# Kernel tuning notes

Hardware: AMD Instinct MI355X
Metric: run time of the kernel (lower is better)

The kernel has to match this reference:

```python
import jax, jax.numpy as jnp
import numpy as np

N = 100000
E = 1600000
H = 128


def setup_inputs() -> dict:
    key = jax.random.key(0)
    ks = jax.random.split(key, 9)
    s = 1.0 / np.sqrt(H)
    x = jax.random.normal(ks[0], (N, H), dtype=jnp.float32)
    edge_index = jax.random.randint(ks[1], (2, E), 0, N, dtype=jnp.int64)
    W1l = jax.random.uniform(ks[2], (H, H), jnp.float32, -s, s)
    b1l = jax.random.uniform(ks[3], (H,), jnp.float32, -s, s)
    W1r = jax.random.uniform(ks[4], (H, H), jnp.float32, -s, s)
    W2l = jax.random.uniform(ks[5], (H, H), jnp.float32, -s, s)
    b2l = jax.random.uniform(ks[6], (H,), jnp.float32, -s, s)
    W2r = jax.random.uniform(ks[7], (H, H), jnp.float32, -s, s)
    return {"x": x, "edge_index": edge_index, "W1l": W1l, "b1l": b1l,
            "W1r": W1r, "W2l": W2l, "b2l": b2l, "W2r": W2r}


def _sage(x, src, dst, Wl, bl, Wr):
    # mean-aggregate source features at destination nodes (PyG SAGEConv default)
    n = x.shape[0]
    msg = x[src]                                             # [E, H]
    summed = jax.ops.segment_sum(msg, dst, num_segments=n)   # [N, H]
    cnt = jax.ops.segment_sum(jnp.ones((src.shape[0],), x.dtype), dst,
                              num_segments=n)
    mean = summed / jnp.maximum(cnt, 1.0)[:, None]
    # out = lin_l(mean) + lin_r(x); bias only on lin_l
    return mean @ Wl.T + bl + x @ Wr.T


def reference(x, edge_index, W1l, b1l, W1r, W2l, b2l, W2r):
    src, dst = edge_index[0], edge_index[1]
    h1 = jax.nn.relu(_sage(x, src, dst, W1l, b1l, W1r))
    return _sage(h1, src, dst, W2l, b2l, W2r)
```

## Files before the change

kernel.cpp:

```cpp
#include <hip/hip_runtime.h>

#define N_NODES 100000
#define N_EDGES 1600000
#define H 128

#define NB 391
#define P1_EPB 4096
#define P1_BLOCKS ((N_EDGES + P1_EPB - 1) / P1_EPB)
#define P2_CAP 6144

typedef unsigned short u16;
typedef unsigned int u32;
typedef short bf16x8 __attribute__((ext_vector_type(8)));
typedef float f32x4 __attribute__((ext_vector_type(4)));

static __device__ __forceinline__ u16 f2bf(float f) {
    u32 u = __float_as_uint(f);
    u += 0x7fffu + ((u >> 16) & 1u);
    return (u16)(u >> 16);
}


__global__ void zero_ints(int* __restrict__ p, int n) {
    int i = blockIdx.x * blockDim.x + threadIdx.x;
    if (i < n) p[i] = 0;
}

__global__ __launch_bounds__(1024) void bucket_count(
    const int* __restrict__ dst, int* __restrict__ gcount)
{
    __shared__ int s_cnt[NB];
    const int t = threadIdx.x;
    const int e0 = blockIdx.x * P1_EPB;
    const int ecnt = min(P1_EPB, N_EDGES - e0);
    for (int i = t; i < NB; i += 1024) s_cnt[i] = 0;
    __syncthreads();
    for (int i = t; i < ecnt; i += 1024)
        atomicAdd(&s_cnt[dst[e0 + i] >> 8], 1);
    __syncthreads();
    for (int i = t; i < NB; i += 1024)
        if (s_cnt[i] > 0) atomicAdd(&gcount[i], s_cnt[i]);
}

__global__ __launch_bounds__(512) void bucket_scan(
    const int* __restrict__ gcount, int* __restrict__ bstart, int* __restrict__ bcur)
{
    __shared__ int s[512];
    int t = threadIdx.x;
    int v = (t < NB) ? gcount[t] : 0;
    s[t] = v;
    __syncthreads();
    for (int off = 1; off < 512; off <<= 1) {
        int add = (t >= off) ? s[t - off] : 0;
        __syncthreads();
        s[t] += add;
        __syncthreads();
    }
    if (t < NB) {
        int excl = s[t] - v;
        bstart[t] = excl;
        bcur[t] = excl;
    }
    if (t == NB - 1) bstart[NB] = s[t];
}

__global__ __launch_bounds__(1024) void p1_bin(
    const int* __restrict__ src, const int* __restrict__ dst,
    int* __restrict__ bcur, u32* __restrict__ csrp)
{
    __shared__ int s_cnt[NB];
    __shared__ int s_lstart[NB];
    __shared__ int s_gbase[NB];
    __shared__ int s_scan[512];
    __shared__ u32 s_val[P1_EPB];
    __shared__ u32 s_gaddr[P1_EPB];

    const int t = threadIdx.x;
    const int e0 = blockIdx.x * P1_EPB;
    const int ecnt = min(P1_EPB, N_EDGES - e0);

    for (int i = t; i < NB; i += 1024) s_cnt[i] = 0;
    __syncthreads();
    for (int i = t; i < ecnt; i += 1024)
        atomicAdd(&s_cnt[dst[e0 + i] >> 8], 1);
    __syncthreads();

    int v = (t < NB) ? s_cnt[t] : 0;
    if (t < 512) s_scan[t] = v;
    __syncthreads();
    for (int off = 1; off < 512; off <<= 1) {
        int add = (t < 512 && t >= off) ? s_scan[t - off] : 0;
        __syncthreads();
        if (t < 512) s_scan[t] += add;
        __syncthreads();
    }
    if (t < NB) {
        int ls = s_scan[t] - v;
        s_lstart[t] = ls;
        s_gbase[t] = (v > 0) ? atomicAdd(&bcur[t], v) : 0;
        s_cnt[t] = ls;
    }
    __syncthreads();

    for (int i = t; i < ecnt; i += 1024) {
        int d = dst[e0 + i];
        int s = src[e0 + i];
        int b = d >> 8;
        int slot = atomicAdd(&s_cnt[b], 1);
        s_val[slot]   = ((u32)(d & 255) << 17) | (u32)s;
        s_gaddr[slot] = (u32)(s_gbase[b] + (slot - s_lstart[b]));
    }
    __syncthreads();
    for (int i = t; i < ecnt; i += 1024)
        csrp[s_gaddr[i]] = s_val[i];
}

__global__ __launch_bounds__(1024) void p2_scatter(
    const int* __restrict__ bstart, int* __restrict__ rowstart,
    int* __restrict__ deg, int* __restrict__ csr)
{
    __shared__ u32 s_in[P2_CAP];
    __shared__ u32 s_out[P2_CAP];
    __shared__ int s_cnt[256];
    __shared__ int s_loc[256];
    const int b = blockIdx.x;
    const int t = threadIdx.x;
    const int n0 = b << 8;
    const int s0 = bstart[b];
    const int s1 = bstart[b + 1];
    const int cnt = s1 - s0;

    if (t < 256) s_cnt[t] = 0;
    __syncthreads();
    for (int i = t; i < cnt; i += 1024) {
        u32 p = (u32)csr[s0 + i];
        s_in[i] = p;
        atomicAdd(&s_cnt[p >> 17], 1);
    }
    __syncthreads();
    if (t < 256) s_loc[t] = s_cnt[t];
    __syncthreads();
    for (int off = 1; off < 256; off <<= 1) {
        int add = (t < 256 && t >= off) ? s_loc[t - off] : 0;
        __syncthreads();
        if (t < 256) s_loc[t] += add;
        __syncthreads();
    }
    if (t < 256) {
        int node = n0 + t;
        int excl = s_loc[t] - s_cnt[t];
        if (node < N_NODES) {
            rowstart[node] = s0 + excl;
            deg[node]      = s_cnt[t];
        }
        s_loc[t] = excl;
    }
    __syncthreads();
    for (int i = t; i < cnt; i += 1024) {
        u32 p = s_in[i];
        int pos = atomicAdd(&s_loc[p >> 17], 1);
        s_out[pos] = p & 0x1FFFFu;
    }
    __syncthreads();
    for (int i = t; i < cnt; i += 1024)
        csr[s0 + i] = (int)s_out[i];
}


__global__ __launch_bounds__(256) void cast_x(const float* __restrict__ in,
                                              u16* __restrict__ out) {
    int i = blockIdx.x * 256 + threadIdx.x;
    const float4 v0 = *(const float4*)(in + (size_t)i * 8);
    const float4 v1 = *(const float4*)(in + (size_t)i * 8 + 4);
    u16 o[8];
    o[0]=f2bf(v0.x); o[1]=f2bf(v0.y); o[2]=f2bf(v0.z); o[3]=f2bf(v0.w);
    o[4]=f2bf(v1.x); o[5]=f2bf(v1.y); o[6]=f2bf(v1.z); o[7]=f2bf(v1.w);
    *(bf16x8*)(out + (size_t)i * 8) = *(bf16x8*)o;
}

__global__ __launch_bounds__(256) void cast_w(const float* __restrict__ w1l,
                                              const float* __restrict__ w1r,
                                              const float* __restrict__ w2l,
                                              const float* __restrict__ w2r,
                                              u16* __restrict__ out) {
    int i = blockIdx.x * 256 + threadIdx.x;
    int mat = i >> 14, idx = i & 16383;
    const float* s = (mat == 0) ? w1l : (mat == 1) ? w1r : (mat == 2) ? w2l : w2r;
    out[i] = f2bf(s[idx]);
}


__global__ __launch_bounds__(256) void agg_bf16(
    const u16* __restrict__ xin, const int* __restrict__ csr,
    const int* __restrict__ rowstart, const int* __restrict__ deg,
    u16* __restrict__ mout)
{
    int w = (blockIdx.x * blockDim.x + threadIdx.x) >> 6;
    if (w >= N_NODES) return;
    int lane = threadIdx.x & 63;
    int beg = __builtin_amdgcn_readfirstlane(rowstart[w]);
    int d   = __builtin_amdgcn_readfirstlane(deg[w]);
    const u16* base = xin + (lane << 1);

    float ax[8], ay[8];
#pragma unroll
    for (int u = 0; u < 8; ++u) { ax[u] = 0.f; ay[u] = 0.f; }

    int i = 0;
    for (; i + 8 <= d; i += 8) {
        int s[8];
#pragma unroll
        for (int u = 0; u < 8; ++u) s[u] = csr[beg + i + u];
#pragma unroll
        for (int u = 0; u < 8; ++u) {
            u32 v = *(const u32*)(base + ((size_t)s[u] << 7));
            ax[u] += __uint_as_float(v << 16);
            ay[u] += __uint_as_float(v & 0xffff0000u);
        }
    }
    if (i < d) {
        int cnt = d - i;
        int s[8];
#pragma unroll
        for (int u = 0; u < 8; ++u) s[u] = csr[beg + i + ((u < cnt) ? u : 0)];
#pragma unroll
        for (int u = 0; u < 8; ++u) {
            u32 v = *(const u32*)(base + ((size_t)s[u] << 7));
            if (u < cnt) {
                ax[u] += __uint_as_float(v << 16);
                ay[u] += __uint_as_float(v & 0xffff0000u);
            }
        }
    }

#pragma unroll
    for (int u = 0; u < 4; ++u) { ax[u] += ax[u + 4]; ay[u] += ay[u + 4]; }
    ax[0] += ax[2]; ay[0] += ay[2];
    ax[1] += ax[3]; ay[1] += ay[3];
    ax[0] += ax[1]; ay[0] += ay[1];

    float inv = 1.f / (float)(d > 0 ? d : 1);
    u32 packed = (u32)f2bf(ax[0] * inv) | ((u32)f2bf(ay[0] * inv) << 16);
    *(u32*)(mout + ((size_t)w << 7) + (lane << 1)) = packed;
}

__global__ __launch_bounds__(256) void gemm_mfma4(
    const u16* __restrict__ Ab, const u16* __restrict__ Xb,
    const u16* __restrict__ Wlb, const float* __restrict__ bl,
    const u16* __restrict__ Wrb, void* __restrict__ outp, int relu_bf16)
{
    __shared__ u16 lds[32768];
    const int t  = threadIdx.x;
    const int wv = t >> 6;
    const int l  = t & 63;
    const int lr = l & 15;
    const int lq = l >> 4;
    const int r0 = blockIdx.x * 128;

    bf16x8 bwl[2][4], bwr[2][4];
#pragma unroll
    for (int ct = 0; ct < 2; ++ct) {
        const u16* wl = Wlb + (size_t)(wv * 32 + ct * 16 + lr) * H + lq * 8;
        const u16* wr = Wrb + (size_t)(wv * 32 + ct * 16 + lr) * H + lq * 8;
#pragma unroll
        for (int k0 = 0; k0 < 4; ++k0) {
            bwl[ct][k0] = *(const bf16x8*)(wl + k0 * 32);
            bwr[ct][k0] = *(const bf16x8*)(wr + k0 * 32);
        }
    }
    float bv[2] = { bl[wv * 32 + lr], bl[wv * 32 + 16 + lr] };

    const char* ag = (const char*)(Ab + (size_t)r0 * H);
    const char* xg = (const char*)(Xb + (size_t)r0 * H);
#pragma unroll
    for (int c = 0; c < 8; ++c) {
        int boff = wv * 8192 + c * 1024;
        __builtin_amdgcn_global_load_lds(
            (const u32*)(ag + boff + (l << 4)), (u32*)&lds[boff >> 1], 16, 0, 0);
        __builtin_amdgcn_global_load_lds(
            (const u32*)(xg + boff + (l << 4)), (u32*)&lds[(32768 + boff) >> 1], 16, 0, 0);
    }
    __syncthreads();

    f32x4 acc[8][2];
#pragma unroll
    for (int rt = 0; rt < 8; ++rt) {
        bf16x8 af[4], xf[4];
#pragma unroll
        for (int k0 = 0; k0 < 4; ++k0) {
            int idx = (rt * 16 + lr) * 128 + k0 * 32 + lq * 8;
            af[k0] = *(const bf16x8*)&lds[idx];
            xf[k0] = *(const bf16x8*)&lds[16384 + idx];
        }
#pragma unroll
        for (int ct = 0; ct < 2; ++ct) {
            f32x4 a = (f32x4)0.f;
#pragma unroll
            for (int k0 = 0; k0 < 4; ++k0) {
                a = __builtin_amdgcn_mfma_f32_16x16x32_bf16(af[k0], bwl[ct][k0], a, 0, 0, 0);
                a = __builtin_amdgcn_mfma_f32_16x16x32_bf16(xf[k0], bwr[ct][k0], a, 0, 0, 0);
            }
            acc[rt][ct] = a;
        }
    }
    __syncthreads();

    if (relu_bf16) {
#pragma unroll
        for (int rt = 0; rt < 8; ++rt)
#pragma unroll
        for (int ct = 0; ct < 2; ++ct)
#pragma unroll
        for (int r = 0; r < 4; ++r)
            lds[(rt * 16 + lq * 4 + r) * 128 + wv * 32 + ct * 16 + lr] =
                f2bf(fmaxf(acc[rt][ct][r] + bv[ct], 0.f));
        __syncthreads();
        u16* ob = (u16*)outp;
#pragma unroll
        for (int c = 0; c < 8; ++c) {
            int eoff = c * 2048 + t * 8;
            int row = r0 + (eoff >> 7);
            if (row < N_NODES)
                *(bf16x8*)(ob + (size_t)r0 * H + eoff) = *(const bf16x8*)&lds[eoff];
        }
    } else {
        float* of = (float*)lds;
#pragma unroll
        for (int rt = 0; rt < 8; ++rt)
#pragma unroll
        for (int ct = 0; ct < 2; ++ct)
#pragma unroll
        for (int r = 0; r < 4; ++r)
            of[(rt * 16 + lq * 4 + r) * 128 + wv * 32 + ct * 16 + lr] =
                acc[rt][ct][r] + bv[ct];
        __syncthreads();
        float* og = (float*)outp;
#pragma unroll
        for (int c = 0; c < 16; ++c) {
            int eoff = c * 1024 + t * 4;
            int row = r0 + (eoff >> 7);
            if (row < N_NODES)
                *(float4*)(og + (size_t)r0 * H + eoff) = *(const float4*)&of[eoff];
        }
    }
}


extern "C" void kernel_launch(void* const* d_in, const int* in_sizes, int n_in,
                              void* d_out, int out_size, void* d_ws, size_t ws_size,
                              hipStream_t stream) {
    const float* x   = (const float*)d_in[0];
    const int*   ei  = (const int*)d_in[1];
    const float* W1l = (const float*)d_in[2];
    const float* b1l = (const float*)d_in[3];
    const float* W1r = (const float*)d_in[4];
    const float* W2l = (const float*)d_in[5];
    const float* b2l = (const float*)d_in[6];
    const float* W2r = (const float*)d_in[7];

    const int* src = ei;
    const int* dst = ei + N_EDGES;

    u16* xb       = (u16*)d_ws;
    u16* mb       = xb + (size_t)N_NODES * H;
    int* deg      = (int*)(mb + (size_t)N_NODES * H);
    int* rowstart = deg + N_NODES;
    int* wslot    = rowstart + N_NODES;
    int* csr      = wslot + N_NODES;
    int* gcount   = csr + N_EDGES;
    int* bstart   = gcount + NB;
    int* bcur     = bstart + NB + 1;
    u16* Wb       = (u16*)wslot;
    u16* W1lb = Wb;
    u16* W1rb = Wb + 16384;
    u16* W2lb = Wb + 32768;
    u16* W2rb = Wb + 49152;

    zero_ints<<<(NB + 255) / 256, 256, 0, stream>>>(gcount, NB);
    bucket_count<<<P1_BLOCKS, 1024, 0, stream>>>(dst, gcount);
    bucket_scan<<<1, 512, 0, stream>>>(gcount, bstart, bcur);
    p1_bin<<<P1_BLOCKS, 1024, 0, stream>>>(src, dst, bcur, (u32*)csr);
    p2_scatter<<<NB, 1024, 0, stream>>>(bstart, rowstart, deg, csr);

    cast_w<<<65536 / 256, 256, 0, stream>>>(W1l, W1r, W2l, W2r, Wb);
    cast_x<<<(N_NODES * H / 8) / 256, 256, 0, stream>>>(x, xb);

    const int gemm_grid = (N_NODES + 127) / 128;

    agg_bf16<<<(N_NODES + 3) / 4, 256, 0, stream>>>(xb, csr, rowstart, deg, mb);
    gemm_mfma4<<<gemm_grid, 256, 0, stream>>>(mb, xb, W1lb, b1l, W1rb, xb, 1);

    agg_bf16<<<(N_NODES + 3) / 4, 256, 0, stream>>>(xb, csr, rowstart, deg, mb);
    gemm_mfma4<<<gemm_grid, 256, 0, stream>>>(mb, xb, W2lb, b2l, W2rb, d_out, 0);
}
```

Before: 239.9 us.

## Aggregate neighbors with 16-byte loads across four lane groups

The mean-aggregation kernel now splits each wavefront into four 16-lane groups. Each lane loads 8 bf16 features (16 bytes) instead of 4 bytes, and each group handles different edges. Partial sums are combined with cross-lane shuffles before one group writes the result. This aims to cut the number of memory instructions per gathered row and raise edge-level parallelism, at the cost of shuffle reductions and more registers per lane.

```diff
diff --git a/kernel.cpp b/kernel.cpp
--- a/kernel.cpp
+++ b/kernel.cpp
@@ -12,12 +12,21 @@
 typedef unsigned short u16;
 typedef unsigned int u32;
 typedef short bf16x8 __attribute__((ext_vector_type(8)));
+typedef u32 u32x4 __attribute__((ext_vector_type(4)));
 typedef float f32x4 __attribute__((ext_vector_type(4)));
 
 static __device__ __forceinline__ u16 f2bf(float f) {
     u32 u = __float_as_uint(f);
     u += 0x7fffu + ((u >> 16) & 1u);
     return (u16)(u >> 16);
+}
+
+static __device__ __forceinline__ void acc8(float* a, u32x4 r) {
+#pragma unroll
+    for (int c = 0; c < 4; ++c) {
+        a[2 * c]     += __uint_as_float(r[c] << 16);
+        a[2 * c + 1] += __uint_as_float(r[c] & 0xffff0000u);
+    }
 }
 
 
@@ -189,7 +198,6 @@
     out[i] = f2bf(s[idx]);
 }
 
-
 __global__ __launch_bounds__(256) void agg_bf16(
     const u16* __restrict__ xin, const int* __restrict__ csr,
     const int* __restrict__ rowstart, const int* __restrict__ deg,
@@ -198,50 +206,52 @@
     int w = (blockIdx.x * blockDim.x + threadIdx.x) >> 6;
     if (w >= N_NODES) return;
     int lane = threadIdx.x & 63;
+    int g = lane >> 4;
+    int s = lane & 15;
     int beg = __builtin_amdgcn_readfirstlane(rowstart[w]);
     int d   = __builtin_amdgcn_readfirstlane(deg[w]);
-    const u16* base = xin + (lane << 1);
-
-    float ax[8], ay[8];
-#pragma unroll
-    for (int u = 0; u < 8; ++u) { ax[u] = 0.f; ay[u] = 0.f; }
+    const u16* base = xin + s * 8;
+
+    float a0[8], a1[8];
+#pragma unroll
+    for (int c = 0; c < 8; ++c) { a0[c] = 0.f; a1[c] = 0.f; }
 
     int i = 0;
-    for (; i + 8 <= d; i += 8) {
-        int s[8];
-#pragma unroll
-        for (int u = 0; u < 8; ++u) s[u] = csr[beg + i + u];
-#pragma unroll
-        for (int u = 0; u < 8; ++u) {
-            u32 v = *(const u32*)(base + ((size_t)s[u] << 7));
-            ax[u] += __uint_as_float(v << 16);
-            ay[u] += __uint_as_float(v & 0xffff0000u);
-        }
+    for (; i + 16 <= d; i += 16) {
+        int e0 = beg + i + g * 4;
+        int j0 = csr[e0], j1 = csr[e0 + 1], j2 = csr[e0 + 2], j3 = csr[e0 + 3];
+        u32x4 r0 = *(const u32x4*)(base + ((size_t)j0 << 7));
+        u32x4 r1 = *(const u32x4*)(base + ((size_t)j1 << 7));
+        u32x4 r2 = *(const u32x4*)(base + ((size_t)j2 << 7));
+        u32x4 r3 = *(const u32x4*)(base + ((size_t)j3 << 7));
+        acc8(a0, r0); acc8(a1, r1); acc8(a0, r2); acc8(a1, r3);
     }
     if (i < d) {
-        int cnt = d - i;
-        int s[8];
-#pragma unroll
-        for (int u = 0; u < 8; ++u) s[u] = csr[beg + i + ((u < cnt) ? u : 0)];
-#pragma unroll
-        for (int u = 0; u < 8; ++u) {
-            u32 v = *(const u32*)(base + ((size_t)s[u] << 7));
-            if (u < cnt) {
-                ax[u] += __uint_as_float(v << 16);
-                ay[u] += __uint_as_float(v & 0xffff0000u);
-            }
-        }
-    }
-
-#pragma unroll
-    for (int u = 0; u < 4; ++u) { ax[u] += ax[u + 4]; ay[u] += ay[u + 4]; }
-    ax[0] += ax[2]; ay[0] += ay[2];
-    ax[1] += ax[3]; ay[1] += ay[3];
-    ax[0] += ax[1]; ay[0] += ay[1];
-
-    float inv = 1.f / (float)(d > 0 ? d : 1);
-    u32 packed = (u32)f2bf(ax[0] * inv) | ((u32)f2bf(ay[0] * inv) << 16);
-    *(u32*)(mout + ((size_t)w << 7) + (lane << 1)) = packed;
+#pragma unroll
+        for (int j = 0; j < 4; ++j) {
+            int e = i + g * 4 + j;
+            int ec = beg + ((e < d) ? e : 0);
+            int jj = csr[ec];
+            u32x4 r = *(const u32x4*)(base + ((size_t)jj << 7));
+            if (e < d) { if (j & 1) acc8(a1, r); else acc8(a0, r); }
+        }
+    }
+
+#pragma unroll
+    for (int c = 0; c < 8; ++c) a0[c] += a1[c];
+#pragma unroll
+    for (int c = 0; c < 8; ++c) {
+        a0[c] += __shfl_xor(a0[c], 16, 64);
+        a0[c] += __shfl_xor(a0[c], 32, 64);
+    }
+
+    if (g == 0) {
+        float inv = 1.f / (float)(d > 0 ? d : 1);
+        u16 o[8];
+#pragma unroll
+        for (int c = 0; c < 8; ++c) o[c] = f2bf(a0[c] * inv);
+        *(bf16x8*)(mout + ((size_t)w << 7) + s * 8) = *(bf16x8*)o;
+    }
 }
 
 __global__ __launch_bounds__(256) void gemm_mfma4(
```

Measured after the change: 246.4 us. 1.03x slower.
